# Kernel optimization log

Hardware: AMD Instinct MI355X
Metric: run time of the kernel (lower is better)

## Reference

```python
import jax, jax.numpy as jnp
import numpy as np


def setup_inputs() -> dict:
    key = jax.random.key(0)
    k1, k2, k3, k4, k5 = jax.random.split(key, 5)
    V, D = 100000, 128
    B, C, K = 16384, 10, 10
    # Xavier-uniform init bound for (V, D) embedding: sqrt(6/(V+D))
    bound = float(np.sqrt(6.0 / (V + D)))
    return {
        "context": jax.random.randint(k1, (B, C), 0, V),
        "target": jax.random.randint(k2, (B,), 0, V),
        "neg_targets": jax.random.randint(k3, (B, K), 0, V),
        "W_in": jax.random.uniform(k4, (V, D), jnp.float32, -bound, bound),
        "W_out": jax.random.uniform(k5, (V, D), jnp.float32, -bound, bound),
    }


def reference(context, target, neg_targets, W_in, W_out):
    # h: (B, D) mean of context embeddings
    h = W_in[context].mean(axis=1)
    # positive score: (B,)
    pos_emb = W_out[target]                      # (B, D)
    pos_score = jnp.sum(h * pos_emb, axis=1)     # (B,)
    pos_loss = jax.nn.log_sigmoid(pos_score)
    # negative scores: (B, K) via batched dot
    neg_emb = W_out[neg_targets]                 # (B, K, D)
    neg_score = jnp.einsum("bkd,bd->bk", neg_emb, h)
    neg_loss = jax.nn.log_sigmoid(-neg_score).sum(axis=1)
    return -(pos_loss + neg_loss).mean()
```

## Files before the change

### kernel.cpp

```cpp
#include <hip/hip_runtime.h>
#include <math.h>

#define WAVES_PER_BLOCK 4

__device__ __forceinline__ float log_sigmoid_fast(float x) {
    return fminf(x, 0.0f) - __logf(1.0f + __expf(-fabsf(x)));
}

__global__ __launch_bounds__(256) void cbow_partial_kernel(
    const int* __restrict__ context,
    const int* __restrict__ target,
    const int* __restrict__ neg_targets,
    const float* __restrict__ W_in,
    const float* __restrict__ W_out,
    float* __restrict__ partial,
    int B)
{
    const int lane = threadIdx.x & 63;
    const int wave = threadIdx.x >> 6;
    const int half = lane >> 5;
    const int l    = lane & 31;

    int b = (blockIdx.x * WAVES_PER_BLOCK + wave) * 2 + half;
    const bool valid = (b < B);
    if (b >= B) b = 0;

    const float4* __restrict__ Win4  = (const float4*)W_in;
    const float4* __restrict__ Wout4 = (const float4*)W_out;

    int cidx[10], nidx[10], tidx;
    #pragma unroll
    for (int c = 0; c < 10; ++c) cidx[c] = context[b * 10 + c];
    tidx = target[b];
    #pragma unroll
    for (int k = 0; k < 10; ++k) nidx[k] = neg_targets[b * 10 + k];

    float4 cr[10];
    #pragma unroll
    for (int c = 0; c < 10; ++c) cr[c] = Win4[(size_t)cidx[c] * 32 + l];
    float4 orow[11];
    orow[0] = Wout4[(size_t)tidx * 32 + l];
    #pragma unroll
    for (int k = 0; k < 10; ++k) orow[1 + k] = Wout4[(size_t)nidx[k] * 32 + l];

    float4 h = {0.f, 0.f, 0.f, 0.f};
    #pragma unroll
    for (int c = 0; c < 10; ++c) {
        h.x += cr[c].x; h.y += cr[c].y; h.z += cr[c].z; h.w += cr[c].w;
    }
    h.x *= 0.1f; h.y *= 0.1f; h.z *= 0.1f; h.w *= 0.1f;

    float s[11];
    #pragma unroll
    for (int i = 0; i < 11; ++i) {
        const float4 v = orow[i];
        s[i] = h.x * v.x + h.y * v.y + h.z * v.z + h.w * v.w;
    }

    #pragma unroll
    for (int off = 16; off > 0; off >>= 1) {
        #pragma unroll
        for (int i = 0; i < 11; ++i)
            s[i] += __shfl_xor(s[i], off, 64);
    }

    float loss = log_sigmoid_fast(s[0]);
    #pragma unroll
    for (int k = 0; k < 10; ++k)
        loss += log_sigmoid_fast(-s[1 + k]);
    if (!valid) loss = 0.f;

    loss += __shfl_xor(loss, 32, 64);

    __shared__ float wsum[WAVES_PER_BLOCK];
    if (lane == 0) wsum[wave] = loss;
    __syncthreads();
    if (threadIdx.x == 0) {
        float t = 0.f;
        #pragma unroll
        for (int w = 0; w < WAVES_PER_BLOCK; ++w) t += wsum[w];
        partial[blockIdx.x] = t;
    }
}

__global__ __launch_bounds__(256) void reduce_partials_kernel(
    const float* __restrict__ partial, int n, float* __restrict__ out, float scale)
{
    __shared__ float sm[4];
    float t = 0.f;
    for (int i = threadIdx.x; i < n; i += 256) t += partial[i];
    #pragma unroll
    for (int off = 32; off > 0; off >>= 1) t += __shfl_xor(t, off, 64);
    const int lane = threadIdx.x & 63;
    const int wave = threadIdx.x >> 6;
    if (lane == 0) sm[wave] = t;
    __syncthreads();
    if (threadIdx.x == 0) {
        out[0] = (sm[0] + sm[1] + sm[2] + sm[3]) * scale;
    }
}

extern "C" void kernel_launch(void* const* d_in, const int* in_sizes, int n_in,
                              void* d_out, int out_size, void* d_ws, size_t ws_size,
                              hipStream_t stream) {
    const int* context     = (const int*)d_in[0];
    const int* target      = (const int*)d_in[1];
    const int* neg_targets = (const int*)d_in[2];
    const float* W_in      = (const float*)d_in[3];
    const float* W_out     = (const float*)d_in[4];
    float* out = (float*)d_out;

    const int B = in_sizes[1];
    const int elems_per_block = 2 * WAVES_PER_BLOCK;
    const int nblocks = (B + elems_per_block - 1) / elems_per_block;

    float* partial = (float*)d_ws;

    cbow_partial_kernel<<<nblocks, 256, 0, stream>>>(
        context, target, neg_targets, W_in, W_out, partial, B);

    reduce_partials_kernel<<<1, 256, 0, stream>>>(
        partial, nblocks, out, -1.0f / (float)B);
}
```

Baseline: 34.19 us.

## Map one batch row per wavefront with scalar indices and float2 loads

Each wavefront now handles one batch element instead of two half-waves each handling one, so every lane loads a float2 rather than a float4 from each embedding row. The index loads are made wave-uniform with readfirstlane, which lets row addresses live in scalar registers. The shuffle reduction gains one step across all 64 lanes, the cross-half shuffle is dropped, and the grid doubles in block count. This is meant to cut vector register pressure and address arithmetic, at the cost of narrower memory transactions per lane and twice as many waves.

```diff
diff --git a/kernel.cpp b/kernel.cpp
--- a/kernel.cpp
+++ b/kernel.cpp
@@ -17,48 +17,45 @@
     int B)
 {
     const int lane = threadIdx.x & 63;
-    const int wave = threadIdx.x >> 6;
-    const int half = lane >> 5;
-    const int l    = lane & 31;
+    const int wave = __builtin_amdgcn_readfirstlane(threadIdx.x >> 6);
+    int b = blockIdx.x * WAVES_PER_BLOCK + wave;
+    const bool valid = (b < B);
+    if (!valid) b = 0;
 
-    int b = (blockIdx.x * WAVES_PER_BLOCK + wave) * 2 + half;
-    const bool valid = (b < B);
-    if (b >= B) b = 0;
-
-    const float4* __restrict__ Win4  = (const float4*)W_in;
-    const float4* __restrict__ Wout4 = (const float4*)W_out;
+    const float2* __restrict__ Win2  = (const float2*)W_in;
+    const float2* __restrict__ Wout2 = (const float2*)W_out;
 
     int cidx[10], nidx[10], tidx;
     #pragma unroll
-    for (int c = 0; c < 10; ++c) cidx[c] = context[b * 10 + c];
-    tidx = target[b];
+    for (int c = 0; c < 10; ++c)
+        cidx[c] = __builtin_amdgcn_readfirstlane(context[b * 10 + c]);
+    tidx = __builtin_amdgcn_readfirstlane(target[b]);
     #pragma unroll
-    for (int k = 0; k < 10; ++k) nidx[k] = neg_targets[b * 10 + k];
+    for (int k = 0; k < 10; ++k)
+        nidx[k] = __builtin_amdgcn_readfirstlane(neg_targets[b * 10 + k]);
 
-    float4 cr[10];
+    float2 cr[10];
     #pragma unroll
-    for (int c = 0; c < 10; ++c) cr[c] = Win4[(size_t)cidx[c] * 32 + l];
-    float4 orow[11];
-    orow[0] = Wout4[(size_t)tidx * 32 + l];
+    for (int c = 0; c < 10; ++c)
+        cr[c] = Win2[(size_t)cidx[c] * 64 + lane];
+    float2 orow[11];
+    orow[0] = Wout2[(size_t)tidx * 64 + lane];
     #pragma unroll
-    for (int k = 0; k < 10; ++k) orow[1 + k] = Wout4[(size_t)nidx[k] * 32 + l];
+    for (int k = 0; k < 10; ++k)
+        orow[1 + k] = Wout2[(size_t)nidx[k] * 64 + lane];
 
-    float4 h = {0.f, 0.f, 0.f, 0.f};
+    float hx = 0.f, hy = 0.f;
     #pragma unroll
-    for (int c = 0; c < 10; ++c) {
-        h.x += cr[c].x; h.y += cr[c].y; h.z += cr[c].z; h.w += cr[c].w;
-    }
-    h.x *= 0.1f; h.y *= 0.1f; h.z *= 0.1f; h.w *= 0.1f;
+    for (int c = 0; c < 10; ++c) { hx += cr[c].x; hy += cr[c].y; }
+    hx *= 0.1f; hy *= 0.1f;
 
     float s[11];
     #pragma unroll
-    for (int i = 0; i < 11; ++i) {
-        const float4 v = orow[i];
-        s[i] = h.x * v.x + h.y * v.y + h.z * v.z + h.w * v.w;
-    }
+    for (int i = 0; i < 11; ++i)
+        s[i] = hx * orow[i].x + hy * orow[i].y;
 
     #pragma unroll
-    for (int off = 16; off > 0; off >>= 1) {
+    for (int off = 32; off > 0; off >>= 1) {
         #pragma unroll
         for (int i = 0; i < 11; ++i)
             s[i] += __shfl_xor(s[i], off, 64);
@@ -69,8 +66,6 @@
     for (int k = 0; k < 10; ++k)
         loss += log_sigmoid_fast(-s[1 + k]);
     if (!valid) loss = 0.f;
-
-    loss += __shfl_xor(loss, 32, 64);
 
     __shared__ float wsum[WAVES_PER_BLOCK];
     if (lane == 0) wsum[wave] = loss;
@@ -111,8 +106,7 @@
     float* out = (float*)d_out;
 
     const int B = in_sizes[1];
-    const int elems_per_block = 2 * WAVES_PER_BLOCK;
-    const int nblocks = (B + elems_per_block - 1) / elems_per_block;
+    const int nblocks = (B + WAVES_PER_BLOCK - 1) / WAVES_PER_BLOCK;
 
     float* partial = (float*)d_ws;
 
```

Result: slower. 37.51 us (+9.7%).
